# Kernel optimization log

Hardware: AMD Instinct MI355X
Metric: run time of the kernel (lower is better)

## Reference

```python
import jax, jax.numpy as jnp
import numpy as np

B, N, H = 512, 128, 256      # graphs, nodes per graph, hidden
NH, HD = 8, 32               # heads, head dim
DEG = 8
E = B * N * DEG              # 524288 edges
BN_EPS = 1e-5


def setup_inputs() -> dict:
    key = jax.random.key(0)
    ks = jax.random.split(key, 16)

    def w(k, shape):
        return jax.random.normal(k, shape, dtype=jnp.float32) * 0.02

    # intra-graph random edges: base offset per graph, local src/dst in [0, N)
    base = jnp.repeat(jnp.arange(B, dtype=jnp.int32) * N, N * DEG)
    edge_src = base + jax.random.randint(ks[1], (E,), 0, N, dtype=jnp.int32)
    edge_dst = base + jax.random.randint(ks[2], (E,), 0, N, dtype=jnp.int32)

    return {
        "h": jax.random.normal(ks[0], (B * N, H), dtype=jnp.float32),
        "edge_src": edge_src,
        "edge_dst": edge_dst,
        "gin_w1": w(ks[3], (H, H)), "gin_b1": jnp.zeros((H,), jnp.float32),
        "gin_w2": w(ks[4], (H, H)), "gin_b2": jnp.zeros((H,), jnp.float32),
        "attn_in_w": w(ks[5], (3 * H, H)), "attn_in_b": jnp.zeros((3 * H,), jnp.float32),
        "attn_out_w": w(ks[6], (H, H)), "attn_out_b": jnp.zeros((H,), jnp.float32),
        "bn_local_g": jnp.ones((H,), jnp.float32), "bn_local_b": jnp.zeros((H,), jnp.float32),
        "bn_attn_g": jnp.ones((H,), jnp.float32), "bn_attn_b": jnp.zeros((H,), jnp.float32),
        "bn_out_g": jnp.ones((H,), jnp.float32), "bn_out_b": jnp.zeros((H,), jnp.float32),
        "ffn1_w": w(ks[7], (2 * H, H)), "ffn1_b": jnp.zeros((2 * H,), jnp.float32),
        "ffn2_w": w(ks[8], (H, 2 * H)), "ffn2_b": jnp.zeros((H,), jnp.float32),
    }


def _bn(x, g, b):
    # nn.BatchNorm1d training-mode forward: batch stats over node dim, biased var
    mean = jnp.mean(x, axis=0)
    var = jnp.mean(jnp.square(x - mean), axis=0)
    return g * (x - mean) * jax.lax.rsqrt(var + BN_EPS) + b


def _mha(x, in_w, in_b, out_w, out_b):
    # x: [B, N, H]; uniform graphs -> key_padding_mask is all-valid
    qkv = x @ in_w.T + in_b                           # [B, N, 3H]
    q, k, v = jnp.split(qkv, 3, axis=-1)
    def heads(t):
        return t.reshape(B, N, NH, HD).transpose(0, 2, 1, 3)  # [B, NH, N, HD]
    q, k, v = heads(q), heads(k), heads(v)
    scores = jnp.einsum('bhqd,bhkd->bhqk', q, k) / jnp.sqrt(jnp.float32(HD))
    att = jax.nn.softmax(scores, axis=-1)
    o = jnp.einsum('bhqk,bhkd->bhqd', att, v).transpose(0, 2, 1, 3).reshape(B, N, H)
    return o @ out_w.T + out_b


def reference(h, edge_src, edge_dst,
              gin_w1, gin_b1, gin_w2, gin_b2,
              attn_in_w, attn_in_b, attn_out_w, attn_out_b,
              bn_local_g, bn_local_b, bn_attn_g, bn_attn_b, bn_out_g, bn_out_b,
              ffn1_w, ffn1_b, ffn2_w, ffn2_b):
    # --- local GIN branch: (1+eps)*h + sum_{j in N(i)} h_j, eps=0, then 2-layer MLP
    agg = jax.ops.segment_sum(h[edge_src], edge_dst, num_segments=B * N)
    z = h + agg
    h_local = jax.nn.relu(z @ gin_w1.T + gin_b1) @ gin_w2.T + gin_b2
    h_local = _bn(h + h_local, bn_local_g, bn_local_b)

    # --- global attention branch (to_dense_batch is an exact reshape here)
    h_dense = h.reshape(B, N, H)
    h_attn = _mha(h_dense, attn_in_w, attn_in_b, attn_out_w, attn_out_b).reshape(B * N, H)
    h_attn = _bn(h + h_attn, bn_attn_g, bn_attn_b)

    # --- combine + FFN + out norm
    x = h_local + h_attn
    x = x + jax.nn.relu(x @ ffn1_w.T + ffn1_b) @ ffn2_w.T + ffn2_b
    return _bn(x, bn_out_g, bn_out_b)
```

## Files before the change

kernel.cpp:

```cpp
#include <hip/hip_runtime.h>
#include <hip/hip_bf16.h>

#define B_   512
#define N_   128
#define H_   256
#define NH_  8
#define HD_  32
#define DEG_ 8
#define R_   (B_ * N_)
#define E_   (B_ * N_ * DEG_)
#define EPG_ (N_ * DEG_)

typedef unsigned short u16;
typedef unsigned int u32;

typedef __attribute__((ext_vector_type(8))) short s16x8;
typedef __attribute__((ext_vector_type(4))) float f32x4;

__device__ __forceinline__ float b2f(u16 u) {
  union { u32 i; float f; } v;
  v.i = ((u32)u) << 16;
  return v.f;
}
__device__ __forceinline__ u16 f2b(float f) {
  union { float f; u32 u; } v;
  v.f = f;
  u32 r = (v.u + 0x7fffu + ((v.u >> 16) & 1u)) >> 16;
  return (u16)r;
}
__device__ __forceinline__ void ld4b(const u16* p, float* o) {
  ushort4 v = *(const ushort4*)p;
  o[0] = b2f(v.x); o[1] = b2f(v.y); o[2] = b2f(v.z); o[3] = b2f(v.w);
}

__device__ __forceinline__ int tix(int row, int col) {
  return ((row >> 7) << 15) + (((col >> 6) & 3) << 13) + ((row & 127) << 6) +
         (((((col >> 3) & 7) ^ (row & 7))) << 3) + (col & 7);
}

__device__ __forceinline__ void glds16(const u16* g, u16* l) {
  __builtin_amdgcn_global_load_lds(
      (const __attribute__((address_space(1))) void*)g,
      (__attribute__((address_space(3))) void*)l, 16, 0, 0);
}


#define OFF_GW1 0
#define OFF_GB1 65536
#define OFF_GW2 65792
#define OFF_GB2 131328
#define OFF_AIW 131584
#define OFF_AIB 328192
#define OFF_AOW 328960
#define OFF_AOB 394496
#define OFF_F1W 394752
#define OFF_F1B 525824
#define OFF_F2W 526336
#define OFF_F2B 657408
#define W_TOTAL 657664

__global__ void zero_stats(float* __restrict__ st) {
  st[blockIdx.x * 256 + threadIdx.x] = 0.f;
}

__global__ __launch_bounds__(256) void cvt_h(const float* __restrict__ src,
                                             u16* __restrict__ dst) {
  const int e = (blockIdx.x * 256 + threadIdx.x) * 4;
  const float4 v = *(const float4*)(src + e);
  ushort4 o;
  o.x = f2b(v.x); o.y = f2b(v.y); o.z = f2b(v.z); o.w = f2b(v.w);
  *(ushort4*)(dst + tix(e >> 8, e & 255)) = o;
}

__global__ __launch_bounds__(256) void cvt_w(
    const float* s0, const float* s1, const float* s2, const float* s3,
    const float* s4, const float* s5, const float* s6, const float* s7,
    const float* s8, const float* s9, const float* s10, const float* s11,
    u16* __restrict__ dst) {
  const int sizes[12] = {65536, 256, 65536, 256, 196608, 768,
                         65536, 256, 131072, 512, 131072, 256};
  const float* srcs[12] = {s0, s1, s2, s3, s4, s5, s6, s7, s8, s9, s10, s11};
  int gid = (blockIdx.x * 256 + threadIdx.x) * 4;
  if (gid >= W_TOTAL) return;
  int seg = 0, off = gid;
  while (off >= sizes[seg]) { off -= sizes[seg]; seg++; }
  const float4 v = *(const float4*)(srcs[seg] + off);
  ushort4 o;
  o.x = f2b(v.x); o.y = f2b(v.y); o.z = f2b(v.z); o.w = f2b(v.w);
  *(ushort4*)(dst + gid) = o;
}

#define SROWS_ 32

__global__ __launch_bounds__(256) void agg_kernel(
    const u16* __restrict__ h, const int* __restrict__ esrc,
    const int* __restrict__ edst, u16* __restrict__ z) {
  __shared__ int s_src[EPG_];
  __shared__ int s_cnt[SROWS_];
  __shared__ int s_off[SROWS_ + 1];
  __shared__ int s_pos[SROWS_];
  const int g = blockIdx.x;
  const int r0 = blockIdx.y * SROWS_;
  const int t = threadIdx.x;

  if (t < SROWS_) s_cnt[t] = 0;
  __syncthreads();

  const int ebase = g * EPG_;
  int dl[4], sg[4];
#pragma unroll
  for (int i = 0; i < 4; i++) {
    const int e = ebase + t + i * 256;
    sg[i] = esrc[e];
    dl[i] = edst[e] - g * N_ - r0;
    if ((unsigned)dl[i] < SROWS_) atomicAdd(&s_cnt[dl[i]], 1);
  }
  __syncthreads();
  if (t == 0) {
    int acc = 0;
#pragma unroll
    for (int i = 0; i < SROWS_; i++) { s_off[i] = acc; acc += s_cnt[i]; }
    s_off[SROWS_] = acc;
  }
  __syncthreads();
  if (t < SROWS_) s_pos[t] = s_off[t];
  __syncthreads();
#pragma unroll
  for (int i = 0; i < 4; i++) {
    if ((unsigned)dl[i] < SROWS_) {
      const int slot = atomicAdd(&s_pos[dl[i]], 1);
      s_src[slot] = sg[i];
    }
  }
  __syncthreads();

  const int rg = t >> 5;
  const int c0 = (t & 31) * 8;
  for (int ib = 0; ib < SROWS_; ib += 8) {
    const int i = ib + rg;
    const int row = g * N_ + r0 + i;
    float acc[8];
    {
      const s16x8 v = *(const s16x8*)(h + tix(row, c0));
#pragma unroll
      for (int j = 0; j < 8; j++) acc[j] = b2f((u16)v[j]);
    }
    const int e0 = s_off[i], e1 = s_off[i + 1];
    for (int e = e0; e < e1; e++) {
      const int src = s_src[e];
      const s16x8 v = *(const s16x8*)(h + tix(src, c0));
#pragma unroll
      for (int j = 0; j < 8; j++) acc[j] += b2f((u16)v[j]);
    }
    s16x8 o;
#pragma unroll
    for (int j = 0; j < 8; j++) o[j] = (short)f2b(acc[j]);
    *(s16x8*)(z + tix(row, c0)) = o;
  }
}

template <int NC, int K, int RELU, int RES, int STATS, int ASPLIT, int CMODE>
__global__ __launch_bounds__(256) void gemm_mfma(
    const u16* A, const u16* A2,
    const u16* __restrict__ W, const u16* __restrict__ bias,
    const u16* res, u16* C0, u16* C1, u16* C2,
    float* __restrict__ gsum, float* __restrict__ gsq) {
  __shared__ u16 As[2][64 * 64] __attribute__((aligned(16)));
  __shared__ u16 Bs[2][64 * 64] __attribute__((aligned(16)));

  const int t = threadIdx.x;
  const int wave = t >> 6, lane = t & 63;
  const int wr = wave >> 1, wc = wave & 1;
  const int quad = lane >> 4, ln15 = lane & 15;
  const int row0 = blockIdx.y * 64, col0 = blockIdx.x * 64;

  f32x4 acc[2][2];
#pragma unroll
  for (int i = 0; i < 2; i++)
#pragma unroll
    for (int j = 0; j < 2; j++) acc[i][j] = (f32x4){0.f, 0.f, 0.f, 0.f};

  auto stage = [&](int b, int kt) {
    const u16* Ab;
    int ksl;
    if (ASPLIT) {
      if (kt < 256) { Ab = A; ksl = kt >> 6; } else { Ab = A2; ksl = (kt - 256) >> 6; }
    } else {
      Ab = A; ksl = kt >> 6;
    }
    const u16* abase = Ab + ((size_t)(row0 >> 7) << 15) + (ksl << 13) +
                       ((row0 & 64) << 6);
#pragma unroll
    for (int i = 0; i < 2; i++) {
      const int fid = t + i * 256;
      glds16(abase + fid * 8, &As[b][fid * 8]);
      const int row = fid >> 3;
      const int segp = (fid & 7) ^ (row & 7);
      glds16(W + (size_t)(col0 + row) * K + kt + segp * 8, &Bs[b][fid * 8]);
    }
  };

  stage(0, 0);
  for (int kt = 0; kt < K; kt += 64) {
    const int cur = (kt >> 6) & 1;
    if (kt + 64 < K) {
      stage(cur ^ 1, kt + 64);
      asm volatile("s_waitcnt vmcnt(4)" ::: "memory");
    } else {
      asm volatile("s_waitcnt vmcnt(0)" ::: "memory");
    }
    __builtin_amdgcn_s_barrier();
#pragma unroll
    for (int ks = 0; ks < 64; ks += 32) {
      s16x8 af[2], bf[2];
#pragma unroll
      for (int i = 0; i < 2; i++) {
        const int ra = wr * 32 + i * 16 + ln15;
        af[i] = *(const s16x8*)(
            &As[cur][ra * 64 + ((((ks >> 3) + quad) ^ (ra & 7)) * 8)]);
      }
#pragma unroll
      for (int j = 0; j < 2; j++) {
        const int rb = wc * 32 + j * 16 + ln15;
        bf[j] = *(const s16x8*)(
            &Bs[cur][rb * 64 + ((((ks >> 3) + quad) ^ (rb & 7)) * 8)]);
      }
#pragma unroll
      for (int i = 0; i < 2; i++)
#pragma unroll
        for (int j = 0; j < 2; j++)
          acc[i][j] = __builtin_amdgcn_mfma_f32_16x16x32_bf16(af[i], bf[j], acc[i][j], 0, 0, 0);
    }
    __builtin_amdgcn_s_barrier();
  }

  const int cbase = col0 + wc * 32;
  u16* Cb;
  int coff;
  if (CMODE) {
    const int chunk = col0 >> 8;
    Cb = (chunk == 0) ? C0 : ((chunk == 1) ? C1 : C2);
    coff = (col0 & 255) + wc * 32;
  } else {
    Cb = C0; coff = cbase;
  }

  float bs[2];
#pragma unroll
  for (int j = 0; j < 2; j++) bs[j] = b2f(bias[cbase + j * 16 + ln15]);

  float ssum[2] = {}, ssq[2] = {};
#pragma unroll
  for (int i = 0; i < 2; i++) {
    const int rbase = row0 + wr * 32 + i * 16 + quad * 4;
#pragma unroll
    for (int reg = 0; reg < 4; reg++) {
      const int row = rbase + reg;
#pragma unroll
      for (int j = 0; j < 2; j++) {
        float val = acc[i][j][reg] + bs[j];
        if (RELU) val = fmaxf(val, 0.f);
        if (RES) val += b2f(res[tix(row, cbase + j * 16 + ln15)]);
        Cb[tix(row, coff + j * 16 + ln15)] = f2b(val);
        if (STATS) { ssum[j] += val; ssq[j] += val * val; }
      }
    }
  }

  if (STATS) {
#pragma unroll
    for (int j = 0; j < 2; j++) {
      float s = ssum[j];
      s += __shfl_xor(s, 16);
      s += __shfl_xor(s, 32);
      float q = ssq[j];
      q += __shfl_xor(q, 16);
      q += __shfl_xor(q, 32);
      if (lane < 16) {
        atomicAdd(&gsum[cbase + j * 16 + lane], s);
        atomicAdd(&gsq[cbase + j * 16 + lane], q);
      }
    }
  }
}

__global__ __launch_bounds__(256) void qkv_mfma(
    const u16* A, const u16* __restrict__ W, const u16* __restrict__ bias,
    u16* Cq, u16* Ck, u16* Cv) {
  __shared__ u16 As[2][64 * 64] __attribute__((aligned(16)));
  __shared__ u16 Bs[2][3 * 64 * 64] __attribute__((aligned(16)));

  const int t = threadIdx.x;
  const int wave = t >> 6, lane = t & 63;
  const int wr = wave >> 1, wc = wave & 1;
  const int quad = lane >> 4, ln15 = lane & 15;
  const int row0 = blockIdx.y * 64, col0 = blockIdx.x * 64;

  f32x4 acc[3][2][2];
#pragma unroll
  for (int o = 0; o < 3; o++)
#pragma unroll
    for (int i = 0; i < 2; i++)
#pragma unroll
      for (int j = 0; j < 2; j++) acc[o][i][j] = (f32x4){0.f, 0.f, 0.f, 0.f};

  auto stage = [&](int b, int kt) {
    const u16* abase = A + ((size_t)(row0 >> 7) << 15) + ((kt >> 6) << 13) +
                       ((row0 & 64) << 6);
#pragma unroll
    for (int i = 0; i < 2; i++) {
      const int fid = t + i * 256;
      glds16(abase + fid * 8, &As[b][fid * 8]);
    }
#pragma unroll
    for (int o = 0; o < 3; o++)
#pragma unroll
      for (int i = 0; i < 2; i++) {
        const int fid = t + i * 256;
        const int row = fid >> 3;
        const int segp = (fid & 7) ^ (row & 7);
        glds16(W + (size_t)(o * 256 + col0 + row) * 256 + kt + segp * 8,
               &Bs[b][o * 4096 + fid * 8]);
      }
  };

  stage(0, 0);
  for (int kt = 0; kt < 256; kt += 64) {
    const int cur = (kt >> 6) & 1;
    if (kt + 64 < 256) {
      stage(cur ^ 1, kt + 64);
      asm volatile("s_waitcnt vmcnt(8)" ::: "memory");
    } else {
      asm volatile("s_waitcnt vmcnt(0)" ::: "memory");
    }
    __builtin_amdgcn_s_barrier();
#pragma unroll
    for (int ks = 0; ks < 64; ks += 32) {
      s16x8 af[2];
#pragma unroll
      for (int i = 0; i < 2; i++) {
        const int ra = wr * 32 + i * 16 + ln15;
        af[i] = *(const s16x8*)(
            &As[cur][ra * 64 + ((((ks >> 3) + quad) ^ (ra & 7)) * 8)]);
      }
#pragma unroll
      for (int o = 0; o < 3; o++) {
        s16x8 bf[2];
#pragma unroll
        for (int j = 0; j < 2; j++) {
          const int rb = wc * 32 + j * 16 + ln15;
          bf[j] = *(const s16x8*)(
              &Bs[cur][o * 4096 + rb * 64 + ((((ks >> 3) + quad) ^ (rb & 7)) * 8)]);
        }
#pragma unroll
        for (int i = 0; i < 2; i++)
#pragma unroll
          for (int j = 0; j < 2; j++)
            acc[o][i][j] = __builtin_amdgcn_mfma_f32_16x16x32_bf16(af[i], bf[j], acc[o][i][j], 0, 0, 0);
      }
    }
    __builtin_amdgcn_s_barrier();
  }

  const int cbase = col0 + wc * 32;
#pragma unroll
  for (int o = 0; o < 3; o++) {
    u16* Co = (o == 0) ? Cq : ((o == 1) ? Ck : Cv);
    float bs[2];
#pragma unroll
    for (int j = 0; j < 2; j++) bs[j] = b2f(bias[o * 256 + cbase + j * 16 + ln15]);
#pragma unroll
    for (int i = 0; i < 2; i++) {
      const int rbase = row0 + wr * 32 + i * 16 + quad * 4;
#pragma unroll
      for (int reg = 0; reg < 4; reg++) {
        const int row = rbase + reg;
#pragma unroll
        for (int j = 0; j < 2; j++)
          Co[tix(row, cbase + j * 16 + ln15)] = f2b(acc[o][i][j][reg] + bs[j]);
      }
    }
  }
}

template <int CHUNKS, int RES_LDS, int COMBINE>
__global__ __launch_bounds__(256, 2) void fused_mlp(
    const u16* A, const u16* Ara,
    const u16* __restrict__ W1, const u16* __restrict__ b1,
    const u16* __restrict__ W2, const u16* __restrict__ b2,
    const u16* resg, u16* C, const float* __restrict__ st,
    float* __restrict__ gsum, float* __restrict__ gsq) {
  __shared__ u16 xs[4 * 64 * 64] __attribute__((aligned(16)));
  __shared__ u16 tc[64 * 128] __attribute__((aligned(16)));
  __shared__ u16 Wst[2][128 * 64] __attribute__((aligned(16)));

  const int t = threadIdx.x;
  const int wave = t >> 6, lane = t & 63;
  const int wr = wave >> 1, wc = wave & 1;
  const int quad = lane >> 4, ln15 = lane & 15;
  const int row0 = blockIdx.x * 64;
  const int K2 = CHUNKS * 128;

  if (COMBINE) {
    float* cf = (float*)tc;
#pragma unroll
    for (int k = 0; k < 4; k++) cf[k * 256 + t] = st[1536 + k * 256 + t];
    __syncthreads();
    const size_t tbase = ((size_t)(row0 >> 7) << 15) + ((row0 & 64) << 6);
#pragma unroll
    for (int i = 0; i < 8; i++) {
      const int gid = t + i * 256;
      const int kstep = gid >> 9;
      const int fid = gid & 511;
      const size_t addr = tbase + kstep * 8192 + fid * 8;
      const s16x8 rl = *(const s16x8*)(A + addr);
      const s16x8 ra = *(const s16x8*)(Ara + addr);
      const int seg = (fid & 7) ^ ((fid >> 3) & 7);
      const int col = kstep * 64 + seg * 8;
      const float4 al0 = *(const float4*)(cf + col);
      const float4 al1 = *(const float4*)(cf + col + 4);
      const float4 bl0 = *(const float4*)(cf + 256 + col);
      const float4 bl1 = *(const float4*)(cf + 256 + col + 4);
      const float4 aa0 = *(const float4*)(cf + 512 + col);
      const float4 aa1 = *(const float4*)(cf + 512 + col + 4);
      const float4 ba0 = *(const float4*)(cf + 768 + col);
      const float4 ba1 = *(const float4*)(cf + 768 + col + 4);
      const float al[8] = {al0.x, al0.y, al0.z, al0.w, al1.x, al1.y, al1.z, al1.w};
      const float bl[8] = {bl0.x, bl0.y, bl0.z, bl0.w, bl1.x, bl1.y, bl1.z, bl1.w};
      const float aa[8] = {aa0.x, aa0.y, aa0.z, aa0.w, aa1.x, aa1.y, aa1.z, aa1.w};
      const float ba[8] = {ba0.x, ba0.y, ba0.z, ba0.w, ba1.x, ba1.y, ba1.z, ba1.w};
      s16x8 o;
#pragma unroll
      for (int j = 0; j < 8; j++)
        o[j] = (short)f2b(al[j] * b2f((u16)rl[j]) + bl[j] +
                          aa[j] * b2f((u16)ra[j]) + ba[j]);
      *(s16x8*)(xs + gid * 8) = o;
    }
    __syncthreads();
  } else {
    const u16* abase = A + ((size_t)(row0 >> 7) << 15) + ((row0 & 64) << 6);
#pragma unroll
    for (int i = 0; i < 8; i++) {
      const int gid = t + i * 256;
      const int kstep = gid >> 9;
      const int fid = gid & 511;
      glds16(abase + kstep * 8192 + fid * 8, xs + gid * 8);
    }
  }

  f32x4 acc2[2][8];
#pragma unroll
  for (int i = 0; i < 2; i++)
#pragma unroll
    for (int j = 0; j < 8; j++) acc2[i][j] = (f32x4){0.f, 0.f, 0.f, 0.f};

  auto tca = [&](int row, int col) {
    const int s0 = col >> 3;
    return row * 128 + (((s0 & 8) | ((s0 ^ row) & 7)) << 3) + (col & 7);
  };

  for (int c = 0; c < CHUNKS; c++) {
    f32x4 acc1[2][4];
#pragma unroll
    for (int i = 0; i < 2; i++)
#pragma unroll
      for (int j = 0; j < 4; j++) acc1[i][j] = (f32x4){0.f, 0.f, 0.f, 0.f};

    auto stage1 = [&](int b, int kt) {
#pragma unroll
      for (int i = 0; i < 4; i++) {
        const int fid = t + i * 256;
        const int row = fid >> 3;
        const int segp = (fid & 7) ^ (row & 7);
        glds16(W1 + (size_t)(c * 128 + row) * 256 + kt + segp * 8,
               &Wst[b][fid * 8]);
      }
    };

    stage1(0, 0);
    for (int kt = 0; kt < 256; kt += 64) {
      const int cur = (kt >> 6) & 1;
      if (kt + 64 < 256) {
        stage1(cur ^ 1, kt + 64);
        asm volatile("s_waitcnt vmcnt(4)" ::: "memory");
      } else {
        asm volatile("s_waitcnt vmcnt(0)" ::: "memory");
      }
      __builtin_amdgcn_s_barrier();
#pragma unroll
      for (int ks = 0; ks < 64; ks += 32) {
        s16x8 af[2], bf[4];
#pragma unroll
        for (int i = 0; i < 2; i++) {
          const int ra = wr * 32 + i * 16 + ln15;
          af[i] = *(const s16x8*)(
              &xs[(kt >> 6) * 4096 + ra * 64 +
                  ((((ks >> 3) + quad) ^ (ra & 7)) * 8)]);
        }
#pragma unroll
        for (int j = 0; j < 4; j++) {
          const int rb = wc * 64 + j * 16 + ln15;
          bf[j] = *(const s16x8*)(
              &Wst[cur][rb * 64 + ((((ks >> 3) + quad) ^ (rb & 7)) * 8)]);
        }
#pragma unroll
        for (int i = 0; i < 2; i++)
#pragma unroll
          for (int j = 0; j < 4; j++)
            acc1[i][j] = __builtin_amdgcn_mfma_f32_16x16x32_bf16(af[i], bf[j], acc1[i][j], 0, 0, 0);
      }
      __builtin_amdgcn_s_barrier();
    }

    {
      float b1s[4];
#pragma unroll
      for (int j = 0; j < 4; j++)
        b1s[j] = b2f(b1[c * 128 + wc * 64 + j * 16 + ln15]);
#pragma unroll
      for (int i = 0; i < 2; i++)
#pragma unroll
        for (int reg = 0; reg < 4; reg++) {
          const int rowl = wr * 32 + i * 16 + quad * 4 + reg;
#pragma unroll
          for (int j = 0; j < 4; j++) {
            const int coll = wc * 64 + j * 16 + ln15;
            tc[tca(rowl, coll)] = f2b(fmaxf(acc1[i][j][reg] + b1s[j], 0.f));
          }
        }
    }
    __syncthreads();

    for (int ks2 = 0; ks2 < 2; ks2++) {
#pragma unroll
      for (int i = 0; i < 8; i++) {
        const int fid = t + i * 256;
        const int row = fid >> 3;
        const int segp = (fid & 7) ^ (row & 7);
        glds16(W2 + (size_t)row * K2 + c * 128 + ks2 * 64 + segp * 8,
               &Wst[0][fid * 8]);
      }
      asm volatile("s_waitcnt vmcnt(0)" ::: "memory");
      __builtin_amdgcn_s_barrier();
#pragma unroll
      for (int ksl = 0; ksl < 64; ksl += 32) {
        s16x8 af[2], bf[8];
#pragma unroll
        for (int i = 0; i < 2; i++) {
          const int ra = wr * 32 + i * 16 + ln15;
          af[i] = *(const s16x8*)(&tc[tca(ra, ks2 * 64 + ksl + quad * 8)]);
        }
#pragma unroll
        for (int j = 0; j < 8; j++) {
          const int rb = wc * 128 + j * 16 + ln15;
          bf[j] = *(const s16x8*)(
              &Wst[0][rb * 64 + ((((ksl >> 3) + quad) ^ (rb & 7)) * 8)]);
        }
#pragma unroll
        for (int i = 0; i < 2; i++)
#pragma unroll
          for (int j = 0; j < 8; j++)
            acc2[i][j] = __builtin_amdgcn_mfma_f32_16x16x32_bf16(af[i], bf[j], acc2[i][j], 0, 0, 0);
      }
      __builtin_amdgcn_s_barrier();
    }
  }

  float bs2[8];
#pragma unroll
  for (int j = 0; j < 8; j++)
    bs2[j] = b2f(b2[wc * 128 + j * 16 + ln15]);

  float ssum[8] = {}, ssq[8] = {};
#pragma unroll
  for (int i = 0; i < 2; i++) {
#pragma unroll
    for (int reg = 0; reg < 4; reg++) {
      const int rowl = wr * 32 + i * 16 + quad * 4 + reg;
      const int row = row0 + rowl;
#pragma unroll
      for (int j = 0; j < 8; j++) {
        const int col = wc * 128 + j * 16 + ln15;
        float val = acc2[i][j][reg] + bs2[j];
        if (RES_LDS) {
          val += b2f(xs[(col >> 6) * 4096 + rowl * 64 +
                        ((((col >> 3) & 7) ^ (rowl & 7)) << 3) + (col & 7)]);
        } else {
          val += b2f(resg[tix(row, col)]);
        }
        C[tix(row, col)] = f2b(val);
        ssum[j] += val; ssq[j] += val * val;
      }
    }
  }

#pragma unroll
  for (int j = 0; j < 8; j++) {
    float s = ssum[j];
    s += __shfl_xor(s, 16);
    s += __shfl_xor(s, 32);
    float q = ssq[j];
    q += __shfl_xor(q, 16);
    q += __shfl_xor(q, 32);
    if (lane < 16) {
      atomicAdd(&gsum[wc * 128 + j * 16 + lane], s);
      atomicAdd(&gsq[wc * 128 + j * 16 + lane], q);
    }
  }
}

__global__ __launch_bounds__(256) void attn_mfma(
    const u16* q, const u16* __restrict__ k,
    const u16* __restrict__ v, u16* o) {
  __shared__ u16 lds[21760] __attribute__((aligned(16)));
  u16* Vt = lds;
  u16* Qs = lds + 4352;
  u16* Ks = lds + 4352 + 5120;
  u16* P  = lds + 4352;

  const int g = blockIdx.x >> 3;
  const int hd = blockIdx.x & 7;
  const int t = threadIdx.x;
  const int wave = t >> 6, lane = t & 63;
  const int quad = lane >> 4, ln15 = lane & 15;
  const int strip = wave * 32;
  const float scale = 0.1767766952966369f;

#pragma unroll
  for (int i = 0; i < 4; i++) {
    const int fid = t + i * 256;
    const int row = fid >> 3;
    const int seg = fid & 7;
    const int gidx = tix(g * N_ + row, hd * HD_ + seg * 4);
    const ushort4 qv = *(const ushort4*)(q + gidx);
    const ushort4 kv = *(const ushort4*)(k + gidx);
    const ushort4 vv = *(const ushort4*)(v + gidx);
    ushort4 qs;
    qs.x = f2b(b2f(qv.x) * scale); qs.y = f2b(b2f(qv.y) * scale);
    qs.z = f2b(b2f(qv.z) * scale); qs.w = f2b(b2f(qv.w) * scale);
    *(ushort4*)(Qs + row * 40 + seg * 4) = qs;
    *(ushort4*)(Ks + row * 40 + seg * 4) = kv;
    Vt[(seg * 4 + 0) * 136 + row] = vv.x;
    Vt[(seg * 4 + 1) * 136 + row] = vv.y;
    Vt[(seg * 4 + 2) * 136 + row] = vv.z;
    Vt[(seg * 4 + 3) * 136 + row] = vv.w;
  }
  __syncthreads();

  s16x8 af[2], bf[8];
#pragma unroll
  for (int mi = 0; mi < 2; mi++)
    af[mi] = *(const s16x8*)(Qs + (strip + mi * 16 + ln15) * 40 + quad * 8);
#pragma unroll
  for (int nj = 0; nj < 8; nj++)
    bf[nj] = *(const s16x8*)(Ks + (nj * 16 + ln15) * 40 + quad * 8);

  f32x4 acc[2][8];
#pragma unroll
  for (int mi = 0; mi < 2; mi++)
#pragma unroll
    for (int nj = 0; nj < 8; nj++)
      acc[mi][nj] = __builtin_amdgcn_mfma_f32_16x16x32_bf16(
          af[mi], bf[nj], (f32x4){0.f, 0.f, 0.f, 0.f}, 0, 0, 0);

  __syncthreads();

#pragma unroll
  for (int mi = 0; mi < 2; mi++) {
#pragma unroll
    for (int reg = 0; reg < 4; reg++) {
      float mx = acc[mi][0][reg];
#pragma unroll
      for (int j = 1; j < 8; j++) mx = fmaxf(mx, acc[mi][j][reg]);
      mx = fmaxf(mx, __shfl_xor(mx, 1));
      mx = fmaxf(mx, __shfl_xor(mx, 2));
      mx = fmaxf(mx, __shfl_xor(mx, 4));
      mx = fmaxf(mx, __shfl_xor(mx, 8));
      float e[8], s = 0.f;
#pragma unroll
      for (int j = 0; j < 8; j++) { e[j] = __expf(acc[mi][j][reg] - mx); s += e[j]; }
      s += __shfl_xor(s, 1);
      s += __shfl_xor(s, 2);
      s += __shfl_xor(s, 4);
      s += __shfl_xor(s, 8);
      const float inv = 1.f / s;
      const int prow = strip + mi * 16 + quad * 4 + reg;
#pragma unroll
      for (int j = 0; j < 8; j++)
        P[prow * 136 + j * 16 + ln15] = f2b(e[j] * inv);
    }
  }
  __syncthreads();

  f32x4 acc2[2][2];
#pragma unroll
  for (int mi = 0; mi < 2; mi++)
#pragma unroll
    for (int nj = 0; nj < 2; nj++) acc2[mi][nj] = (f32x4){0.f, 0.f, 0.f, 0.f};
#pragma unroll
  for (int kt = 0; kt < 4; kt++) {
    s16x8 paf[2], vbf[2];
#pragma unroll
    for (int mi = 0; mi < 2; mi++)
      paf[mi] = *(const s16x8*)(P + (strip + mi * 16 + ln15) * 136 + kt * 32 + quad * 8);
#pragma unroll
    for (int nj = 0; nj < 2; nj++)
      vbf[nj] = *(const s16x8*)(Vt + (nj * 16 + ln15) * 136 + kt * 32 + quad * 8);
#pragma unroll
    for (int mi = 0; mi < 2; mi++)
#pragma unroll
      for (int nj = 0; nj < 2; nj++)
        acc2[mi][nj] = __builtin_amdgcn_mfma_f32_16x16x32_bf16(
            paf[mi], vbf[nj], acc2[mi][nj], 0, 0, 0);
  }

#pragma unroll
  for (int mi = 0; mi < 2; mi++)
#pragma unroll
    for (int nj = 0; nj < 2; nj++)
#pragma unroll
      for (int reg = 0; reg < 4; reg++) {
        const int row = strip + mi * 16 + quad * 4 + reg;
        o[tix(g * N_ + row, hd * HD_ + nj * 16 + ln15)] =
            f2b(acc2[mi][nj][reg]);
      }
}

__global__ void bn_finalize(const float* __restrict__ sum,
                            const float* __restrict__ sq,
                            const float* __restrict__ g,
                            const float* __restrict__ bb,
                            float* __restrict__ a, float* __restrict__ b) {
  const int c = threadIdx.x;
  const float mean = sum[c] * (1.f / R_);
  const float var = fmaxf(sq[c] * (1.f / R_) - mean * mean, 0.f);
  const float ai = g[c] * rsqrtf(var + 1e-5f);
  a[c] = ai;
  b[c] = bb[c] - mean * ai;
}

__global__ __launch_bounds__(256) void final_kernel(
    const u16* __restrict__ y, const float* __restrict__ st,
    float* __restrict__ out) {
  const int e = (blockIdx.x * 256 + threadIdx.x) * 4;
  const int col = e & 255;
  float y4[4];
  ld4b(y + tix(e >> 8, col), y4);
  const float* ao = st + 2560;
  const float* bo = st + 2816;
  float4 o;
  o.x = ao[col + 0] * y4[0] + bo[col + 0];
  o.y = ao[col + 1] * y4[1] + bo[col + 1];
  o.z = ao[col + 2] * y4[2] + bo[col + 2];
  o.w = ao[col + 3] * y4[3] + bo[col + 3];
  *(float4*)(out + e) = o;
}

extern "C" void kernel_launch(void* const* d_in, const int* in_sizes, int n_in,
                              void* d_out, int out_size, void* d_ws, size_t ws_size,
                              hipStream_t stream) {
  const float* h = (const float*)d_in[0];
  const int* esrc = (const int*)d_in[1];
  const int* edst = (const int*)d_in[2];
  const float* bn_local_g = (const float*)d_in[11];
  const float* bn_local_b = (const float*)d_in[12];
  const float* bn_attn_g = (const float*)d_in[13];
  const float* bn_attn_b = (const float*)d_in[14];
  const float* bn_out_g = (const float*)d_in[15];
  const float* bn_out_b = (const float*)d_in[16];

  const size_t RH = (size_t)R_ * H_;
  float* stats = (float*)d_ws;
  u16* WB = (u16*)((char*)d_ws + 65536);
  u16* Hb = (u16*)((char*)d_ws + 65536 + 2097152);
  u16* S1 = Hb + RH;
  u16* S2 = S1 + RH;
  u16* OD = (u16*)d_out;
  float* outf = (float*)d_out;

  zero_stats<<<12, 256, 0, stream>>>(stats);
  cvt_h<<<(int)(RH / 4 / 256), 256, 0, stream>>>(h, Hb);
  cvt_w<<<(W_TOTAL / 4 + 255) / 256, 256, 0, stream>>>(
      (const float*)d_in[3], (const float*)d_in[4], (const float*)d_in[5],
      (const float*)d_in[6], (const float*)d_in[7], (const float*)d_in[8],
      (const float*)d_in[9], (const float*)d_in[10], (const float*)d_in[17],
      (const float*)d_in[18], (const float*)d_in[19], (const float*)d_in[20], WB);

  qkv_mfma<<<dim3(4, 1024), 256, 0, stream>>>(
      Hb, WB + OFF_AIW, WB + OFF_AIB, S1, S2, OD);
  attn_mfma<<<B_ * NH_, 256, 0, stream>>>(S1, S2, OD, S1);
  gemm_mfma<256, 256, 0, 1, 1, 0, 0><<<dim3(4, 1024), 256, 0, stream>>>(
      S1, nullptr, WB + OFF_AOW, WB + OFF_AOB, Hb, S2, nullptr, nullptr,
      stats + 512, stats + 768);
  agg_kernel<<<dim3(B_, 4), 256, 0, stream>>>(Hb, esrc, edst, OD);
  fused_mlp<2, 0, 0><<<1024, 256, 0, stream>>>(
      OD, nullptr, WB + OFF_GW1, WB + OFF_GB1, WB + OFF_GW2, WB + OFF_GB2,
      Hb, OD, nullptr, stats + 0, stats + 256);

  bn_finalize<<<1, 256, 0, stream>>>(stats + 0, stats + 256, bn_local_g,
                                     bn_local_b, stats + 1536, stats + 1792);
  bn_finalize<<<1, 256, 0, stream>>>(stats + 512, stats + 768, bn_attn_g,
                                     bn_attn_b, stats + 2048, stats + 2304);

  fused_mlp<4, 1, 1><<<1024, 256, 0, stream>>>(
      OD, S2, WB + OFF_F1W, WB + OFF_F1B, WB + OFF_F2W, WB + OFF_F2B,
      nullptr, S1, stats, stats + 1024, stats + 1280);

  bn_finalize<<<1, 256, 0, stream>>>(stats + 1024, stats + 1280, bn_out_g,
                                     bn_out_b, stats + 2560, stats + 2816);
  final_kernel<<<(int)(RH / 4 / 256), 256, 0, stream>>>(S1, stats, outf);
}
```

Before: 535.8 us.

## Fuse GIN neighbor aggregation into MLP kernel and fold BN finalize into consumers

The GIN aggregation now runs inside the first fused MLP kernel: it builds per-tile CSR lists in shared memory, gathers neighbor rows and writes the summed tile straight into the swizzled LDS input buffer. This removes the separate agg kernel and the global round-trip of z. The three conversion/zero kernels are merged into one prep launch, and the bn_finalize launches are folded into the combine stage and the final kernel, which recompute the scale and shift per element. The cost is a serialized gather phase at the start of each MLP block and some redundant per-thread BN arithmetic.

New measurement: 546.6 us. 1.02x slower.

```diff
diff --git a/kernel.cpp b/kernel.cpp
--- a/kernel.cpp
+++ b/kernel.cpp
@@ -59,103 +59,33 @@
 #define OFF_F2B 657408
 #define W_TOTAL 657664
 
-__global__ void zero_stats(float* __restrict__ st) {
-  st[blockIdx.x * 256 + threadIdx.x] = 0.f;
-}
-
-__global__ __launch_bounds__(256) void cvt_h(const float* __restrict__ src,
-                                             u16* __restrict__ dst) {
-  const int e = (blockIdx.x * 256 + threadIdx.x) * 4;
-  const float4 v = *(const float4*)(src + e);
-  ushort4 o;
-  o.x = f2b(v.x); o.y = f2b(v.y); o.z = f2b(v.z); o.w = f2b(v.w);
-  *(ushort4*)(dst + tix(e >> 8, e & 255)) = o;
-}
-
-__global__ __launch_bounds__(256) void cvt_w(
+__global__ __launch_bounds__(256) void prep_kernel(
+    const float* __restrict__ hsrc, u16* __restrict__ hdst,
     const float* s0, const float* s1, const float* s2, const float* s3,
     const float* s4, const float* s5, const float* s6, const float* s7,
     const float* s8, const float* s9, const float* s10, const float* s11,
-    u16* __restrict__ dst) {
-  const int sizes[12] = {65536, 256, 65536, 256, 196608, 768,
-                         65536, 256, 131072, 512, 131072, 256};
-  const float* srcs[12] = {s0, s1, s2, s3, s4, s5, s6, s7, s8, s9, s10, s11};
-  int gid = (blockIdx.x * 256 + threadIdx.x) * 4;
-  if (gid >= W_TOTAL) return;
-  int seg = 0, off = gid;
-  while (off >= sizes[seg]) { off -= sizes[seg]; seg++; }
-  const float4 v = *(const float4*)(srcs[seg] + off);
-  ushort4 o;
-  o.x = f2b(v.x); o.y = f2b(v.y); o.z = f2b(v.z); o.w = f2b(v.w);
-  *(ushort4*)(dst + gid) = o;
-}
-
-#define SROWS_ 32
-
-__global__ __launch_bounds__(256) void agg_kernel(
-    const u16* __restrict__ h, const int* __restrict__ esrc,
-    const int* __restrict__ edst, u16* __restrict__ z) {
-  __shared__ int s_src[EPG_];
-  __shared__ int s_cnt[SROWS_];
-  __shared__ int s_off[SROWS_ + 1];
-  __shared__ int s_pos[SROWS_];
-  const int g = blockIdx.x;
-  const int r0 = blockIdx.y * SROWS_;
-  const int t = threadIdx.x;
-
-  if (t < SROWS_) s_cnt[t] = 0;
-  __syncthreads();
-
-  const int ebase = g * EPG_;
-  int dl[4], sg[4];
-#pragma unroll
-  for (int i = 0; i < 4; i++) {
-    const int e = ebase + t + i * 256;
-    sg[i] = esrc[e];
-    dl[i] = edst[e] - g * N_ - r0;
-    if ((unsigned)dl[i] < SROWS_) atomicAdd(&s_cnt[dl[i]], 1);
-  }
-  __syncthreads();
-  if (t == 0) {
-    int acc = 0;
-#pragma unroll
-    for (int i = 0; i < SROWS_; i++) { s_off[i] = acc; acc += s_cnt[i]; }
-    s_off[SROWS_] = acc;
-  }
-  __syncthreads();
-  if (t < SROWS_) s_pos[t] = s_off[t];
-  __syncthreads();
-#pragma unroll
-  for (int i = 0; i < 4; i++) {
-    if ((unsigned)dl[i] < SROWS_) {
-      const int slot = atomicAdd(&s_pos[dl[i]], 1);
-      s_src[slot] = sg[i];
-    }
-  }
-  __syncthreads();
-
-  const int rg = t >> 5;
-  const int c0 = (t & 31) * 8;
-  for (int ib = 0; ib < SROWS_; ib += 8) {
-    const int i = ib + rg;
-    const int row = g * N_ + r0 + i;
-    float acc[8];
-    {
-      const s16x8 v = *(const s16x8*)(h + tix(row, c0));
-#pragma unroll
-      for (int j = 0; j < 8; j++) acc[j] = b2f((u16)v[j]);
-    }
-    const int e0 = s_off[i], e1 = s_off[i + 1];
-    for (int e = e0; e < e1; e++) {
-      const int src = s_src[e];
-      const s16x8 v = *(const s16x8*)(h + tix(src, c0));
-#pragma unroll
-      for (int j = 0; j < 8; j++) acc[j] += b2f((u16)v[j]);
-    }
-    s16x8 o;
-#pragma unroll
-    for (int j = 0; j < 8; j++) o[j] = (short)f2b(acc[j]);
-    *(s16x8*)(z + tix(row, c0)) = o;
+    u16* __restrict__ wdst, float* __restrict__ stats) {
+  const int b = blockIdx.x, t = threadIdx.x;
+  if (b < 16384) {
+    const int e = (b * 256 + t) * 4;
+    const float4 v = *(const float4*)(hsrc + e);
+    ushort4 o;
+    o.x = f2b(v.x); o.y = f2b(v.y); o.z = f2b(v.z); o.w = f2b(v.w);
+    *(ushort4*)(hdst + tix(e >> 8, e & 255)) = o;
+  } else if (b < 16384 + 643) {
+    const int sizes[12] = {65536, 256, 65536, 256, 196608, 768,
+                           65536, 256, 131072, 512, 131072, 256};
+    const float* srcs[12] = {s0, s1, s2, s3, s4, s5, s6, s7, s8, s9, s10, s11};
+    int gid = ((b - 16384) * 256 + t) * 4;
+    if (gid >= W_TOTAL) return;
+    int seg = 0, off = gid;
+    while (off >= sizes[seg]) { off -= sizes[seg]; seg++; }
+    const float4 v = *(const float4*)(srcs[seg] + off);
+    ushort4 o;
+    o.x = f2b(v.x); o.y = f2b(v.y); o.z = f2b(v.z); o.w = f2b(v.w);
+    *(ushort4*)(wdst + gid) = o;
+  } else {
+    stats[(b - (16384 + 643)) * 256 + t] = 0.f;
   }
 }
 
@@ -383,12 +313,15 @@
   }
 }
 
-template <int CHUNKS, int RES_LDS, int COMBINE>
+template <int CHUNKS, int RES_LDS, int COMBINE, int GATHER>
 __global__ __launch_bounds__(256, 2) void fused_mlp(
     const u16* A, const u16* Ara,
+    const int* __restrict__ esrc, const int* __restrict__ edst,
     const u16* __restrict__ W1, const u16* __restrict__ b1,
     const u16* __restrict__ W2, const u16* __restrict__ b2,
     const u16* resg, u16* C, const float* __restrict__ st,
+    const float* __restrict__ bn0g, const float* __restrict__ bn0b,
+    const float* __restrict__ bn1g, const float* __restrict__ bn1b,
     float* __restrict__ gsum, float* __restrict__ gsq) {
   __shared__ u16 xs[4 * 64 * 64] __attribute__((aligned(16)));
   __shared__ u16 tc[64 * 128] __attribute__((aligned(16)));
@@ -401,10 +334,80 @@
   const int row0 = blockIdx.x * 64;
   const int K2 = CHUNKS * 128;
 
-  if (COMBINE) {
+  if (GATHER) {
+    int* s_srcp = (int*)tc;
+    int* s_cntp = (int*)(tc + 2048);
+    int* s_offp = (int*)(tc + 2304);
+    int* s_posp = (int*)(tc + 2560);
+    if (t < 64) s_cntp[t] = 0;
+    __syncthreads();
+    const int g = row0 >> 7;
+    const int r0l = row0 & 64;
+    const int ebase = g * EPG_;
+    int dl[4], sv[4];
+#pragma unroll
+    for (int i = 0; i < 4; i++) {
+      const int e = ebase + t + i * 256;
+      sv[i] = esrc[e];
+      dl[i] = edst[e] - g * N_ - r0l;
+      if ((unsigned)dl[i] < 64u) atomicAdd(&s_cntp[dl[i]], 1);
+    }
+    __syncthreads();
+    if (t == 0) {
+      int a = 0;
+#pragma unroll
+      for (int i = 0; i < 64; i++) { s_offp[i] = a; a += s_cntp[i]; }
+      s_offp[64] = a;
+    }
+    __syncthreads();
+    if (t < 64) s_posp[t] = s_offp[t];
+    __syncthreads();
+#pragma unroll
+    for (int i = 0; i < 4; i++) {
+      if ((unsigned)dl[i] < 64u) {
+        const int slot = atomicAdd(&s_posp[dl[i]], 1);
+        s_srcp[slot] = sv[i];
+      }
+    }
+    __syncthreads();
+    const int rg = t >> 5;
+    const int c0 = (t & 31) * 8;
+    const int panel = c0 >> 6;
+    const int segi = (c0 >> 3) & 7;
+    for (int ib = 0; ib < 64; ib += 8) {
+      const int rowl = ib + rg;
+      float acc[8];
+      {
+        const s16x8 v = *(const s16x8*)(A + tix(row0 + rowl, c0));
+#pragma unroll
+        for (int j = 0; j < 8; j++) acc[j] = b2f((u16)v[j]);
+      }
+      const int e0 = s_offp[rowl], e1 = s_offp[rowl + 1];
+      for (int e = e0; e < e1; e++) {
+        const s16x8 v = *(const s16x8*)(A + tix(s_srcp[e], c0));
+#pragma unroll
+        for (int j = 0; j < 8; j++) acc[j] += b2f((u16)v[j]);
+      }
+      s16x8 o;
+#pragma unroll
+      for (int j = 0; j < 8; j++) o[j] = (short)f2b(acc[j]);
+      *(s16x8*)(xs + panel * 4096 + rowl * 64 + ((segi ^ (rowl & 7)) << 3)) = o;
+    }
+    __syncthreads();
+  } else if (COMBINE) {
     float* cf = (float*)tc;
-#pragma unroll
-    for (int k = 0; k < 4; k++) cf[k * 256 + t] = st[1536 + k * 256 + t];
+    {
+      const float ml = st[t] * (1.f / R_);
+      const float vl = fmaxf(st[256 + t] * (1.f / R_) - ml * ml, 0.f);
+      const float al = bn0g[t] * rsqrtf(vl + 1e-5f);
+      cf[t] = al;
+      cf[256 + t] = bn0b[t] - ml * al;
+      const float ma = st[512 + t] * (1.f / R_);
+      const float va = fmaxf(st[768 + t] * (1.f / R_) - ma * ma, 0.f);
+      const float aa = bn1g[t] * rsqrtf(va + 1e-5f);
+      cf[512 + t] = aa;
+      cf[768 + t] = bn1b[t] - ma * aa;
+    }
     __syncthreads();
     const size_t tbase = ((size_t)(row0 >> 7) << 15) + ((row0 & 64) << 6);
 #pragma unroll
@@ -726,33 +729,31 @@
       }
 }
 
-__global__ void bn_finalize(const float* __restrict__ sum,
-                            const float* __restrict__ sq,
-                            const float* __restrict__ g,
-                            const float* __restrict__ bb,
-                            float* __restrict__ a, float* __restrict__ b) {
-  const int c = threadIdx.x;
-  const float mean = sum[c] * (1.f / R_);
-  const float var = fmaxf(sq[c] * (1.f / R_) - mean * mean, 0.f);
-  const float ai = g[c] * rsqrtf(var + 1e-5f);
-  a[c] = ai;
-  b[c] = bb[c] - mean * ai;
-}
-
 __global__ __launch_bounds__(256) void final_kernel(
     const u16* __restrict__ y, const float* __restrict__ st,
+    const float* __restrict__ bg, const float* __restrict__ bb,
     float* __restrict__ out) {
   const int e = (blockIdx.x * 256 + threadIdx.x) * 4;
   const int col = e & 255;
   float y4[4];
   ld4b(y + tix(e >> 8, col), y4);
-  const float* ao = st + 2560;
-  const float* bo = st + 2816;
+  const float4 s4 = *(const float4*)(st + 1024 + col);
+  const float4 q4 = *(const float4*)(st + 1280 + col);
+  const float4 g4 = *(const float4*)(bg + col);
+  const float4 b4 = *(const float4*)(bb + col);
+  const float ss[4] = {s4.x, s4.y, s4.z, s4.w};
+  const float qq[4] = {q4.x, q4.y, q4.z, q4.w};
+  const float gg[4] = {g4.x, g4.y, g4.z, g4.w};
+  const float bv[4] = {b4.x, b4.y, b4.z, b4.w};
   float4 o;
-  o.x = ao[col + 0] * y4[0] + bo[col + 0];
-  o.y = ao[col + 1] * y4[1] + bo[col + 1];
-  o.z = ao[col + 2] * y4[2] + bo[col + 2];
-  o.w = ao[col + 3] * y4[3] + bo[col + 3];
+  float* ov = (float*)&o;
+#pragma unroll
+  for (int j = 0; j < 4; j++) {
+    const float mean = ss[j] * (1.f / R_);
+    const float var = fmaxf(qq[j] * (1.f / R_) - mean * mean, 0.f);
+    const float a = gg[j] * rsqrtf(var + 1e-5f);
+    ov[j] = a * y4[j] + (bv[j] - mean * a);
+  }
   *(float4*)(out + e) = o;
 }
 
@@ -778,13 +779,13 @@
   u16* OD = (u16*)d_out;
   float* outf = (float*)d_out;
 
-  zero_stats<<<12, 256, 0, stream>>>(stats);
-  cvt_h<<<(int)(RH / 4 / 256), 256, 0, stream>>>(h, Hb);
-  cvt_w<<<(W_TOTAL / 4 + 255) / 256, 256, 0, stream>>>(
+  prep_kernel<<<16384 + 643 + 12, 256, 0, stream>>>(
+      h, Hb,
       (const float*)d_in[3], (const float*)d_in[4], (const float*)d_in[5],
       (const float*)d_in[6], (const float*)d_in[7], (const float*)d_in[8],
       (const float*)d_in[9], (const float*)d_in[10], (const float*)d_in[17],
-      (const float*)d_in[18], (const float*)d_in[19], (const float*)d_in[20], WB);
+      (const float*)d_in[18], (const float*)d_in[19], (const float*)d_in[20],
+      WB, stats);
 
   qkv_mfma<<<dim3(4, 1024), 256, 0, stream>>>(
       Hb, WB + OFF_AIW, WB + OFF_AIB, S1, S2, OD);
@@ -792,21 +793,16 @@
   gemm_mfma<256, 256, 0, 1, 1, 0, 0><<<dim3(4, 1024), 256, 0, stream>>>(
       S1, nullptr, WB + OFF_AOW, WB + OFF_AOB, Hb, S2, nullptr, nullptr,
       stats + 512, stats + 768);
-  agg_kernel<<<dim3(B_, 4), 256, 0, stream>>>(Hb, esrc, edst, OD);
-  fused_mlp<2, 0, 0><<<1024, 256, 0, stream>>>(
-      OD, nullptr, WB + OFF_GW1, WB + OFF_GB1, WB + OFF_GW2, WB + OFF_GB2,
-      Hb, OD, nullptr, stats + 0, stats + 256);
-
-  bn_finalize<<<1, 256, 0, stream>>>(stats + 0, stats + 256, bn_local_g,
-                                     bn_local_b, stats + 1536, stats + 1792);
-  bn_finalize<<<1, 256, 0, stream>>>(stats + 512, stats + 768, bn_attn_g,
-                                     bn_attn_b, stats + 2048, stats + 2304);
-
-  fused_mlp<4, 1, 1><<<1024, 256, 0, stream>>>(
-      OD, S2, WB + OFF_F1W, WB + OFF_F1B, WB + OFF_F2W, WB + OFF_F2B,
-      nullptr, S1, stats, stats + 1024, stats + 1280);
-
-  bn_finalize<<<1, 256, 0, stream>>>(stats + 1024, stats + 1280, bn_out_g,
-                                     bn_out_b, stats + 2560, stats + 2816);
-  final_kernel<<<(int)(RH / 4 / 256), 256, 0, stream>>>(S1, stats, outf);
-}
+  fused_mlp<2, 0, 0, 1><<<1024, 256, 0, stream>>>(
+      Hb, nullptr, esrc, edst,
+      WB + OFF_GW1, WB + OFF_GB1, WB + OFF_GW2, WB + OFF_GB2,
+      Hb, OD, nullptr, nullptr, nullptr, nullptr, nullptr,
+      stats + 0, stats + 256);
+  fused_mlp<4, 1, 1, 0><<<1024, 256, 0, stream>>>(
+      OD, S2, nullptr, nullptr,
+      WB + OFF_F1W, WB + OFF_F1B, WB + OFF_F2W, WB + OFF_F2B,
+      nullptr, S1, stats, bn_local_g, bn_local_b, bn_attn_g, bn_attn_b,
+      stats + 1024, stats + 1280);
+  final_kernel<<<(int)(RH / 4 / 256), 256, 0, stream>>>(
+      S1, stats, bn_out_g, bn_out_b, outf);
+}
```
